# Kernel optimization log

Hardware: AMD Instinct MI355X
Metric: run time of the kernel (lower is better)

The kernel has to match this reference:

```python
import jax, jax.numpy as jnp
import numpy as np

IMAGE_SIZE = (256, 704)
FEATURE_SIZE = (32, 88)
XBOUND = (-54.0, 54.0, 0.3)
YBOUND = (-54.0, 54.0, 0.3)
ZBOUND = (-10.0, 10.0, 20.0)
DBOUND = (1.0, 60.0, 1.0)


def _grid_params():
    bounds = [XBOUND, YBOUND, ZBOUND]
    dx = jnp.array([b[2] for b in bounds], jnp.float32)
    bx = jnp.array([b[0] + b[2] / 2.0 for b in bounds], jnp.float32)
    nx = [int((b[1] - b[0]) / b[2]) for b in bounds]  # [360, 360, 1]
    return dx, bx, nx


def _frustum():
    iH, iW = IMAGE_SIZE
    fH, fW = FEATURE_SIZE
    ds = jnp.arange(DBOUND[0], DBOUND[1], DBOUND[2], dtype=jnp.float32)  # [D]
    D = ds.shape[0]
    xs = jnp.linspace(0.0, iW - 1, fW, dtype=jnp.float32)
    ys = jnp.linspace(0.0, iH - 1, fH, dtype=jnp.float32)
    xs_b = jnp.broadcast_to(xs[None, None, :], (D, fH, fW))
    ys_b = jnp.broadcast_to(ys[None, :, None], (D, fH, fW))
    ds_b = jnp.broadcast_to(ds[:, None, None], (D, fH, fW))
    return jnp.stack([xs_b, ys_b, ds_b], axis=-1)  # [D, fH, fW, 3]


def setup_inputs() -> dict:
    key = jax.random.key(0)
    k1, k2, k3, k4 = jax.random.split(key, 4)
    B, N, C = 2, 6, 80
    fH, fW = FEATURE_SIZE
    D = _frustum().shape[0]  # 59
    feats = jax.random.normal(k1, (B, N, D, fH, fW, C), dtype=jnp.float32)
    img_trans = 0.5 * jax.random.normal(k2, (B, N, 3), dtype=jnp.float32)
    img_scale = 0.9 + 0.2 * jax.random.uniform(k3, (B, N), dtype=jnp.float32)
    # camera-intrinsic-like lidar2img: diag(focal, focal, 1, 1) + small noise,
    # guaranteed well-conditioned so jnp.linalg.inv is stable
    base = jnp.diag(jnp.array([500.0, 500.0, 1.0, 1.0], jnp.float32))
    lidar2img = base[None, None] + 0.1 * jax.random.normal(k4, (B, N, 4, 4), dtype=jnp.float32)
    return {"feats": feats, "img_trans": img_trans, "img_scale": img_scale, "lidar2img": lidar2img}


def reference(feats, img_trans, img_scale, lidar2img):
    B, N, D, H, W, C = feats.shape
    dx, bx, nx = _grid_params()
    NX, NY, NZ = nx
    fr = _frustum()  # [D, H, W, 3]

    # ---- get_geometry (eval mode: no pcd augmentations) ----
    pts = fr[None, None] + img_trans[:, :, None, None, None, :]  # [B,N,D,H,W,3]
    d = pts[..., 2:3]
    xy = pts[..., :2] / img_scale[:, :, None, None, None, None]
    ones = jnp.ones_like(d)
    p4 = jnp.concatenate([xy * d, d, ones], axis=-1)  # [B,N,D,H,W,4]
    img2lidar = jnp.linalg.inv(lidar2img)  # [B,N,4,4]
    geom = jnp.einsum('bnij,bndhwj->bndhwi', img2lidar, p4)[..., :3]

    # ---- bev_pool: voxelize + masked scatter-sum into dense BEV grid ----
    # torch .long() truncates toward zero; float->int astype in jax matches
    vox = ((geom - (bx - dx / 2.0)) / dx).astype(jnp.int32)  # [B,N,D,H,W,3]
    vox = vox.reshape(B, -1, 3)
    x = feats.reshape(B, -1, C)
    mask = ((vox[..., 0] >= 0) & (vox[..., 0] < NX)
            & (vox[..., 1] >= 0) & (vox[..., 1] < NY)
            & (vox[..., 2] >= 0) & (vox[..., 2] < NZ))
    # flat index into [B, Z, X, Y] grid
    flat = (vox[..., 2] * NX + vox[..., 0]) * NY + vox[..., 1]
    flat = flat + jnp.arange(B, dtype=jnp.int32)[:, None] * (NZ * NX * NY)
    flat = jnp.where(mask, flat, 0)  # masked points carry zero features -> harmless
    xm = x * mask[..., None].astype(x.dtype)
    grid = jax.ops.segment_sum(xm.reshape(-1, C), flat.reshape(-1),
                               num_segments=B * NZ * NX * NY)
    grid = grid.reshape(B, NZ, NX, NY, C)
    # bev_pool returns [B, C, Z, X, Y]; cat(unbind(dim=2), 1) -> [B, Z*C, X, Y]
    final = jnp.transpose(grid, (0, 1, 4, 2, 3)).reshape(B, NZ * C, NX, NY)
    return final
```

## Files before the change

### kernel.cpp

```cpp
#include <hip/hip_runtime.h>
#include <math.h>

#define B_ 2
#define N_ 6
#define D_ 59
#define FH 32
#define FW 88
#define C_ 80
#define NX 360
#define NY 360
#define P_PER_B (N_*D_*FH*FW)
#define NPTS (B_*P_PER_B)
#define NCELL (NX*NY)
#define NC (B_*NCELL)
#define NBLK 254
#define NCP (NBLK*1024)
#define OUT4 (B_*C_*NCELL/4)
#define SMAX 32
#define CHK 96
#define MAXCHK (NC/4 + NPTS/CHK)
#define TOTBLK 2048
#define NWAVES (TOTBLK*256/64)

__device__ int   g_code[NPTS];
__device__ __align__(16) int g_cnt[NCP];
__device__ int   g_cur[NC];
__device__ __align__(16) int g_plist[NPTS];
__device__ int   g_total;
__device__ int   g_nS, g_nB;
__device__ int   g_nS2, g_nB2;
__device__ int2  g_cellS[NC];
__device__ int2  g_chunkB[MAXCHK];

__global__ void k_geomz(const float* __restrict__ itrans,
                        const float* __restrict__ iscale,
                        const float* __restrict__ l2i,
                        float* __restrict__ out) {
#pragma clang fp contract(off)
  __shared__ float sinv[B_*N_*16];
  int tid = threadIdx.x;
  int p = blockIdx.x*256 + tid;

  const float4 z4 = make_float4(0.f,0.f,0.f,0.f);
  ((float4*)out)[p] = z4;
  ((float4*)out)[p + NPTS] = z4;
  {
    int u = p + 2*NPTS;
    if (u < OUT4) ((float4*)out)[u] = z4;
  }

  if (tid < B_*N_) {
    int m = tid;
    double a[4][4], inv[4][4];
    for (int r=0;r<4;r++) for (int j=0;j<4;j++){
      a[r][j] = (double)l2i[m*16+r*4+j];
      inv[r][j] = (r==j)?1.0:0.0;
    }
    for (int k=0;k<4;k++){
      int pv=k; double mx=fabs(a[k][k]);
      for (int r=k+1;r<4;r++){ double v=fabs(a[r][k]); if (v>mx){mx=v;pv=r;} }
      if (pv!=k){
        for (int j=0;j<4;j++){
          double t=a[k][j]; a[k][j]=a[pv][j]; a[pv][j]=t;
          t=inv[k][j]; inv[k][j]=inv[pv][j]; inv[pv][j]=t;
        }
      }
      double pi = 1.0/a[k][k];
      for (int j=0;j<4;j++){ a[k][j]*=pi; inv[k][j]*=pi; }
      for (int r=0;r<4;r++) if (r!=k){
        double f=a[r][k];
        for (int j=0;j<4;j++){ a[r][j]-=f*a[k][j]; inv[r][j]-=f*inv[k][j]; }
      }
    }
    for (int r=0;r<4;r++) for (int j=0;j<4;j++)
      sinv[m*16+r*4+j] = (float)inv[r][j];
  }
  __syncthreads();

  int b  = p / P_PER_B;
  int r  = p - b*P_PER_B;
  int n  = r / (D_*FH*FW);
  int r2 = r - n*(D_*FH*FW);
  int d  = r2 / (FH*FW);
  int r3 = r2 - d*(FH*FW);
  int h  = r3 / FW;
  int w  = r3 - h*FW;
  int bn = b*N_ + n;

  float xw = (float)((double)w * (703.0/87.0));
  float yh = (float)((double)h * (255.0/31.0));
  float dd = (float)(d + 1);

  float t0 = itrans[bn*3+0], t1 = itrans[bn*3+1], t2 = itrans[bn*3+2];
  float s  = iscale[bn];

  float px = xw + t0, py = yh + t1, pd = dd + t2;
  float x0 = px / s, x1 = py / s;
  float p0 = x0*pd, p1 = x1*pd, p2 = pd;

  const float* iv = &sinv[bn*16];
  float gx = ((iv[0]*p0 + iv[1]*p1) + iv[2]*p2)  + iv[3]*1.0f;
  float gy = ((iv[4]*p0 + iv[5]*p1) + iv[6]*p2)  + iv[7]*1.0f;
  float gz = ((iv[8]*p0 + iv[9]*p1) + iv[10]*p2) + iv[11]*1.0f;

  int vx = (int)((gx + 54.0f) / 0.3f);
  int vy = (int)((gy + 54.0f) / 0.3f);
  int vz = (int)((gz + 10.0f) / 20.0f);

  bool ok = (vx>=0) & (vx<NX) & (vy>=0) & (vy<NY) & (vz>=0) & (vz<1);
  int code = ok ? (b*NCELL + vx*NY + vy) : -1;
  g_code[p] = code;

  int lane = tid & 63;
  int prev = __shfl_up(code, 1);
  bool leader = (lane == 0) || (code != prev);
  unsigned long long m = __ballot(leader);
  if (leader && code >= 0) {
    unsigned long long above = (lane < 63) ? (m >> (lane+1)) : 0ULL;
    int len = above ? __ffsll(above) : (64 - lane);
    atomicAdd(&g_cnt[code], len);
  }
}

__global__ void __launch_bounds__(1024) k_alloc() {
  int t = threadIdx.x, bid = blockIdx.x;
  int i = bid*1024 + t;
  bool inb = (i < NC);
  int len = inb ? g_cnt[i] : 0;
  if (inb && len) g_cnt[i] = 0;
  int lane = t & 63;

  int pre = len;
  #pragma unroll
  for (int off=1; off<64; off<<=1) {
    int x = __shfl_up(pre, off);
    if (lane >= off) pre += x;
  }
  int wtot = __shfl(pre, 63);
  int wbase = 0;
  if (lane == 63 && wtot > 0) wbase = atomicAdd(&g_total, wtot);
  wbase = __shfl(wbase, 63);
  int base = wbase + pre - len;
  if (inb && len > 0) g_cur[i] = base;

  bool isS = inb && (len > 0) && (len <= SMAX);
  unsigned long long m = __ballot(isS);
  if (m) {
    int ldr = __ffsll((long long)m) - 1;
    int cbase = 0;
    if (lane == ldr) cbase = atomicAdd(&g_nS, (int)__popcll(m));
    cbase = __shfl(cbase, ldr);
    if (isS) {
      int rank = __popcll(m & ((1ULL << lane) - 1ULL));
      g_cellS[cbase + rank] = make_int2(i | (len << 18), base);
    }
  }
  if (inb && len > SMAX) {
    int nch = (len + CHK - 1) / CHK;
    int cb = atomicAdd(&g_nB, nch);
    int sole = (nch == 1) ? 1 : 0;
    for (int k = 0; k < nch; ++k) {
      int clen = min(CHK, len - k*CHK);
      g_chunkB[cb + k] = make_int2(i | (clen << 18) | (sole << 30), base + k*CHK);
    }
  }
}

__global__ void k_fill() {
  int gid = blockIdx.x*256 + threadIdx.x;
  if (gid == 0) { g_nS2 = g_nS; g_nB2 = g_nB; g_nS = 0; g_nB = 0; g_total = 0; }

  int code = g_code[gid];
  int lane = threadIdx.x & 63;
  int prev = __shfl_up(code, 1);
  bool leader = (lane == 0) || (code != prev);
  unsigned long long m = __ballot(leader);
  unsigned long long mask_le = (lane==63) ? ~0ULL : ((1ULL << (lane+1)) - 1ULL);
  int leaderLane = 63 - __clzll(m & mask_le);
  int pos0 = 0;
  if (leader && code >= 0) {
    unsigned long long above = (lane < 63) ? (m >> (lane+1)) : 0ULL;
    int len = above ? __ffsll(above) : (64 - lane);
    pos0 = atomicAdd(&g_cur[code], len);
  }
  pos0 = __shfl(pos0, leaderLane);
  if (code >= 0) g_plist[pos0 + (lane - leaderLane)] = gid;
}

__global__ void __launch_bounds__(256) k_gather(const float* __restrict__ feats,
                                                float* __restrict__ out) {
  const float4* f4 = (const float4*)feats;
  int gtid = blockIdx.x*256 + threadIdx.x;
  int lane = threadIdx.x & 63;

  {
    int nB = g_nB2;
    int wid = gtid >> 6;
    int grp = lane/20;
    int c4 = lane - grp*20;
    bool act = lane < 60;
    for (int it = wid; it < nB; it += NWAVES) {
      int2 e = g_chunkB[it];
      int c    = e.x & 0x3FFFF;
      int clen = (e.x >> 18) & 0x7F;
      int sole = (e.x >> 30) & 1;
      int s0 = e.y;
      int s1 = s0 + clen;
      float ax=0.f, ay=0.f, az=0.f, aw=0.f;
      if (act) {
        #pragma unroll 1
        for (int rr=0; rr<4; ++rr) {
          int j0 = s0 + grp + 24*rr;
          if (j0 >= s1) break;
          int p[8];
          #pragma unroll
          for (int k=0;k<8;++k) p[k] = g_plist[min(j0 + 3*k, NPTS-1)];
          float4 v[8];
          #pragma unroll
          for (int k=0;k<8;++k) v[k] = f4[(size_t)min(max(p[k],0),NPTS-1)*20 + c4];
          #pragma unroll
          for (int k=0;k<8;++k) {
            float sel = (j0 + 3*k < s1) ? 1.f : 0.f;
            ax = fmaf(sel, v[k].x, ax);
            ay = fmaf(sel, v[k].y, ay);
            az = fmaf(sel, v[k].z, az);
            aw = fmaf(sel, v[k].w, aw);
          }
        }
      }
      float bx=__shfl(ax,c4+20), by=__shfl(ay,c4+20), bz=__shfl(az,c4+20), bw=__shfl(aw,c4+20);
      float cx=__shfl(ax,c4+40), cy=__shfl(ay,c4+40), cz=__shfl(az,c4+40), cw=__shfl(aw,c4+40);
      if (lane < 20) {
        ax += bx + cx; ay += by + cy; az += bz + cz; aw += bw + cw;
        int b = c / NCELL;
        int xy = c - b*NCELL;
        float* dst = out + (size_t)(b*C_ + c4*4)*NCELL + xy;
        if (sole) {
          dst[0]       = ax;
          dst[NCELL]   = ay;
          dst[2*NCELL] = az;
          dst[3*NCELL] = aw;
        } else {
          atomicAdd(dst,         ax);
          atomicAdd(dst+NCELL,   ay);
          atomicAdd(dst+2*NCELL, az);
          atomicAdd(dst+3*NCELL, aw);
        }
      }
    }
  }

  {
    int nS = g_nS2;
    int tot = nS*20;
    for (int i = gtid; i < tot; i += TOTBLK*256) {
      int ci = i/20;
      int c4 = i - ci*20;
      int2 e = g_cellS[ci];
      int c   = e.x & 0x3FFFF;
      int len = (e.x >> 18) & 0x7F;
      int o0  = e.y;
      float ax=0.f, ay=0.f, az=0.f, aw=0.f;
      int nb = (len + 7) >> 3;
      for (int bi = 0; bi < nb; ++bi) {
        int base = o0 + bi*8;
        int rem = len - bi*8;
        int p[8];
        #pragma unroll
        for (int k=0;k<8;++k) p[k] = g_plist[min(base+k, NPTS-1)];
        float4 v[8];
        #pragma unroll
        for (int k=0;k<8;++k) {
          int q = min(max(p[k],0), NPTS-1);
          v[k] = f4[(size_t)q*20 + c4];
        }
        #pragma unroll
        for (int k=0;k<8;++k) {
          float sel = (k < rem) ? 1.f : 0.f;
          ax = fmaf(sel, v[k].x, ax);
          ay = fmaf(sel, v[k].y, ay);
          az = fmaf(sel, v[k].z, az);
          aw = fmaf(sel, v[k].w, aw);
        }
      }
      int b = c / NCELL;
      int xy = c - b*NCELL;
      float* dst = out + (size_t)(b*C_ + c4*4)*NCELL + xy;
      dst[0]       = ax;
      dst[NCELL]   = ay;
      dst[2*NCELL] = az;
      dst[3*NCELL] = aw;
    }
  }
}

extern "C" void kernel_launch(void* const* d_in, const int* in_sizes, int n_in,
                              void* d_out, int out_size, void* d_ws, size_t ws_size,
                              hipStream_t stream) {
  const float* feats  = (const float*)d_in[0];
  const float* itrans = (const float*)d_in[1];
  const float* iscale = (const float*)d_in[2];
  const float* l2i    = (const float*)d_in[3];
  float* out = (float*)d_out;

  k_geomz<<<NPTS/256, 256, 0, stream>>>(itrans, iscale, l2i, out);
  k_alloc<<<NBLK, 1024, 0, stream>>>();
  k_fill<<<NPTS/256, 256, 0, stream>>>();
  k_gather<<<TOTBLK, 256, 0, stream>>>(feats, out);
}
```

Baseline: 126.3 us.

## Compact run-length point runs in geometry pass and fill from run list

Each geometry thread now handles four consecutive width points. It run-length encodes their voxel codes locally and appends only the valid runs to a compacted global run list through a wave prefix scan and one atomic per wave. The fill kernel then walks this compact list with a small grid instead of rereading a per-point code array, which removes that array and skips invalid points. In exchange, per-run atomics replace wave-wide run merging, so runs that span threads are no longer merged and atomic counts may rise. The plist order now depends on the atomic append order.

```diff
diff --git a/kernel.cpp b/kernel.cpp
--- a/kernel.cpp
+++ b/kernel.cpp
@@ -11,6 +11,7 @@
 #define NY 360
 #define P_PER_B (N_*D_*FH*FW)
 #define NPTS (B_*P_PER_B)
+#define NT4 (NPTS/4)
 #define NCELL (NX*NY)
 #define NC (B_*NCELL)
 #define NBLK 254
@@ -22,10 +23,11 @@
 #define TOTBLK 2048
 #define NWAVES (TOTBLK*256/64)
 
-__device__ int   g_code[NPTS];
 __device__ __align__(16) int g_cnt[NCP];
 __device__ int   g_cur[NC];
 __device__ __align__(16) int g_plist[NPTS];
+__device__ int2  g_runs[NPTS];
+__device__ int   g_nR, g_nR2;
 __device__ int   g_total;
 __device__ int   g_nS, g_nB;
 __device__ int   g_nS2, g_nB2;
@@ -39,13 +41,12 @@
 #pragma clang fp contract(off)
   __shared__ float sinv[B_*N_*16];
   int tid = threadIdx.x;
-  int p = blockIdx.x*256 + tid;
+  int gid = blockIdx.x*256 + tid;
 
   const float4 z4 = make_float4(0.f,0.f,0.f,0.f);
-  ((float4*)out)[p] = z4;
-  ((float4*)out)[p + NPTS] = z4;
-  {
-    int u = p + 2*NPTS;
+  #pragma unroll
+  for (int u4=0; u4<11; ++u4) {
+    int u = gid + u4*NT4;
     if (u < OUT4) ((float4*)out)[u] = z4;
   }
 
@@ -77,54 +78,84 @@
   }
   __syncthreads();
 
-  int b  = p / P_PER_B;
-  int r  = p - b*P_PER_B;
+  int p0 = gid*4;
+  int b  = p0 / P_PER_B;
+  int r  = p0 - b*P_PER_B;
   int n  = r / (D_*FH*FW);
   int r2 = r - n*(D_*FH*FW);
   int d  = r2 / (FH*FW);
   int r3 = r2 - d*(FH*FW);
   int h  = r3 / FW;
-  int w  = r3 - h*FW;
+  int w0 = r3 - h*FW;
   int bn = b*N_ + n;
 
-  float xw = (float)((double)w * (703.0/87.0));
   float yh = (float)((double)h * (255.0/31.0));
   float dd = (float)(d + 1);
 
   float t0 = itrans[bn*3+0], t1 = itrans[bn*3+1], t2 = itrans[bn*3+2];
-  float s  = iscale[bn];
-
-  float px = xw + t0, py = yh + t1, pd = dd + t2;
-  float x0 = px / s, x1 = py / s;
-  float p0 = x0*pd, p1 = x1*pd, p2 = pd;
+  float sc = iscale[bn];
+
+  float py = yh + t1, pd = dd + t2;
+  float x1 = py / sc;
+  float p1v = x1*pd, p2v = pd;
 
   const float* iv = &sinv[bn*16];
-  float gx = ((iv[0]*p0 + iv[1]*p1) + iv[2]*p2)  + iv[3]*1.0f;
-  float gy = ((iv[4]*p0 + iv[5]*p1) + iv[6]*p2)  + iv[7]*1.0f;
-  float gz = ((iv[8]*p0 + iv[9]*p1) + iv[10]*p2) + iv[11]*1.0f;
-
-  int vx = (int)((gx + 54.0f) / 0.3f);
-  int vy = (int)((gy + 54.0f) / 0.3f);
-  int vz = (int)((gz + 10.0f) / 20.0f);
-
-  bool ok = (vx>=0) & (vx<NX) & (vy>=0) & (vy<NY) & (vz>=0) & (vz<1);
-  int code = ok ? (b*NCELL + vx*NY + vy) : -1;
-  g_code[p] = code;
+  float m1x = iv[1]*p1v, m2x = iv[2]*p2v;
+  float m1y = iv[5]*p1v, m2y = iv[6]*p2v;
+  float m1z = iv[9]*p1v, m2z = iv[10]*p2v;
+
+  int c[4];
+  #pragma unroll
+  for (int k=0; k<4; ++k) {
+    float xw = (float)((double)(w0+k) * (703.0/87.0));
+    float px = xw + t0;
+    float x0 = px / sc;
+    float p0v = x0*pd;
+    float gx = ((iv[0]*p0v + m1x) + m2x) + iv[3]*1.0f;
+    float gy = ((iv[4]*p0v + m1y) + m2y) + iv[7]*1.0f;
+    float gz = ((iv[8]*p0v + m1z) + m2z) + iv[11]*1.0f;
+    int vx = (int)((gx + 54.0f) / 0.3f);
+    int vy = (int)((gy + 54.0f) / 0.3f);
+    int vz = (int)((gz + 10.0f) / 20.0f);
+    bool ok = (vx>=0) & (vx<NX) & (vy>=0) & (vy<NY) & (vz>=0) & (vz<1);
+    c[k] = ok ? (b*NCELL + vx*NY + vy) : -1;
+  }
+
+  int2 runs[4];
+  int rc = 0;
+  {
+    int cur = c[0], st = 0;
+    #pragma unroll
+    for (int k=1; k<4; ++k) {
+      if (c[k] != cur) {
+        if (cur >= 0) runs[rc++] = make_int2(cur | ((k-st) << 18), p0 + st);
+        cur = c[k]; st = k;
+      }
+    }
+    if (cur >= 0) runs[rc++] = make_int2(cur | ((4-st) << 18), p0 + st);
+  }
+  for (int k=0; k<rc; ++k)
+    atomicAdd(&g_cnt[runs[k].x & 0x3FFFF], (runs[k].x >> 18) & 7);
 
   int lane = tid & 63;
-  int prev = __shfl_up(code, 1);
-  bool leader = (lane == 0) || (code != prev);
-  unsigned long long m = __ballot(leader);
-  if (leader && code >= 0) {
-    unsigned long long above = (lane < 63) ? (m >> (lane+1)) : 0ULL;
-    int len = above ? __ffsll(above) : (64 - lane);
-    atomicAdd(&g_cnt[code], len);
-  }
+  int pre = rc;
+  #pragma unroll
+  for (int off=1; off<64; off<<=1) {
+    int x = __shfl_up(pre, off);
+    if (lane >= off) pre += x;
+  }
+  int wtot = __shfl(pre, 63);
+  int wbase = 0;
+  if (lane == 63 && wtot > 0) wbase = atomicAdd(&g_nR, wtot);
+  wbase = __shfl(wbase, 63);
+  int myb = wbase + pre - rc;
+  for (int k=0; k<rc; ++k) g_runs[myb + k] = runs[k];
 }
 
 __global__ void __launch_bounds__(1024) k_alloc() {
   int t = threadIdx.x, bid = blockIdx.x;
   int i = bid*1024 + t;
+  if (bid == 0 && t == 0) { g_nR2 = g_nR; g_nR = 0; }
   bool inb = (i < NC);
   int len = inb ? g_cnt[i] : 0;
   if (inb && len) g_cnt[i] = 0;
@@ -169,22 +200,16 @@
 __global__ void k_fill() {
   int gid = blockIdx.x*256 + threadIdx.x;
   if (gid == 0) { g_nS2 = g_nS; g_nB2 = g_nB; g_nS = 0; g_nB = 0; g_total = 0; }
-
-  int code = g_code[gid];
-  int lane = threadIdx.x & 63;
-  int prev = __shfl_up(code, 1);
-  bool leader = (lane == 0) || (code != prev);
-  unsigned long long m = __ballot(leader);
-  unsigned long long mask_le = (lane==63) ? ~0ULL : ((1ULL << (lane+1)) - 1ULL);
-  int leaderLane = 63 - __clzll(m & mask_le);
-  int pos0 = 0;
-  if (leader && code >= 0) {
-    unsigned long long above = (lane < 63) ? (m >> (lane+1)) : 0ULL;
-    int len = above ? __ffsll(above) : (64 - lane);
-    pos0 = atomicAdd(&g_cur[code], len);
-  }
-  pos0 = __shfl(pos0, leaderLane);
-  if (code >= 0) g_plist[pos0 + (lane - leaderLane)] = gid;
+  int nR = g_nR2;
+  for (int i = gid; i < nR; i += 256*256) {
+    int2 e = g_runs[i];
+    int cell = e.x & 0x3FFFF;
+    int len  = (e.x >> 18) & 7;
+    int pos = atomicAdd(&g_cur[cell], len);
+    #pragma unroll
+    for (int k=0; k<4; ++k)
+      if (k < len) g_plist[pos + k] = e.y + k;
+  }
 }
 
 __global__ void __launch_bounds__(256) k_gather(const float* __restrict__ feats,
@@ -303,8 +328,8 @@
   const float* l2i    = (const float*)d_in[3];
   float* out = (float*)d_out;
 
-  k_geomz<<<NPTS/256, 256, 0, stream>>>(itrans, iscale, l2i, out);
+  k_geomz<<<NT4/256, 256, 0, stream>>>(itrans, iscale, l2i, out);
   k_alloc<<<NBLK, 1024, 0, stream>>>();
-  k_fill<<<NPTS/256, 256, 0, stream>>>();
+  k_fill<<<256, 256, 0, stream>>>();
   k_gather<<<TOTBLK, 256, 0, stream>>>(feats, out);
 }
```

After: 154.6 us. 1.22x slower.
